# Kernel tuning notes

Hardware: AMD Instinct MI355X
Metric: run time of the kernel (lower is better)

Reference implementation:

```python
import jax, jax.numpy as jnp
import numpy as np

N = 50000        # nodes
E = 800000       # edges (avg degree 16)
C_IN = 128
H = 256          # hidden_channels
C_OUT = 128
DEPTH = 4
K = 2            # k_hops -> K+1 = 3 TAGConv weight matrices
L = DEPTH - 1    # residual layers after layer-0 conv
EPS = 1e-5
SLOPE = 0.01     # LeakyReLU default negative slope


def setup_inputs() -> dict:
    key = jax.random.key(0)
    ks = iter(jax.random.split(key, 24))
    s = 0.02
    x = jax.random.normal(next(ks), (N, C_IN), dtype=jnp.float32)
    edge_index = jax.random.randint(next(ks), (2, E), 0, N, dtype=jnp.int64)
    edge_weight = jax.random.uniform(next(ks), (E,), dtype=jnp.float32)
    return {
        'x': x,
        'edge_index': edge_index,
        'edge_weight': edge_weight,
        'W_emb': jax.random.normal(next(ks), (C_IN, H)) * s,
        'b_emb': jnp.zeros((H,), jnp.float32),
        'conv0_W': jax.random.normal(next(ks), (K + 1, H, H)) * s,
        'conv0_b': jnp.zeros((H,), jnp.float32),
        'norm_g': jnp.ones((L, H), jnp.float32),
        'norm_b': jnp.zeros((L, H), jnp.float32),
        'conv_W': jax.random.normal(next(ks), (L, K + 1, H, H)) * s,
        'conv_b': jnp.zeros((L, H), jnp.float32),
        'mlp_W1': jax.random.normal(next(ks), (L, H, 4 * H)) * s,
        'mlp_b1': jnp.zeros((L, 4 * H), jnp.float32),
        'mlp_g': jnp.ones((L, 4 * H), jnp.float32),
        'mlp_bb': jnp.zeros((L, 4 * H), jnp.float32),
        'mlp_W2': jax.random.normal(next(ks), (L, 4 * H, H)) * s,
        'mlp_b2': jnp.zeros((L, H), jnp.float32),
        'W_out': jax.random.normal(next(ks), (H, C_OUT)) * s,
        'b_out': jnp.zeros((C_OUT,), jnp.float32),
    }


def _bn(h, g, b):
    # BatchNorm1d over node dim (training-mode batch statistics)
    m = h.mean(axis=0)
    v = h.var(axis=0)
    return g * (h - m) * jax.lax.rsqrt(v + EPS) + b


def _tagconv(h, src, dst, ew, Ws, b):
    # TAGConv (normalize=False, no self loops): sum_k (A^k h) W_k + b
    out = h @ Ws[0]
    p = h
    for k in range(1, Ws.shape[0]):
        msg = p[src] * ew[:, None]                      # [E, H] gather
        p = jax.ops.segment_sum(msg, dst, num_segments=h.shape[0])
        out = out + p @ Ws[k]
    return out + b


def reference(x, edge_index, edge_weight, W_emb, b_emb, conv0_W, conv0_b,
              norm_g, norm_b, conv_W, conv_b, mlp_W1, mlp_b1, mlp_g, mlp_bb,
              mlp_W2, mlp_b2, W_out, b_out):
    src, dst = edge_index[0], edge_index[1]
    h = x @ W_emb + b_emb                               # x_embed (t=None)
    h = _tagconv(h, src, dst, edge_weight, conv0_W, conv0_b)  # layer-0 conv only
    for l in range(norm_g.shape[0]):                    # res+ blocks
        z = jax.nn.leaky_relu(_bn(h, norm_g[l], norm_b[l]), SLOPE)
        z = _tagconv(z, src, dst, edge_weight, conv_W[l], conv_b[l])
        # pyg MLP [H, 4H, H]: Linear -> BN -> act -> Linear (plain last)
        z = jax.nn.leaky_relu(_bn(z @ mlp_W1[l] + mlp_b1[l], mlp_g[l], mlp_bb[l]), SLOPE)
        z = z @ mlp_W2[l] + mlp_b2[l]
        h = h + z                                       # residual (res=Identity)
    return h @ W_out + b_out
```

## Files before the change

kernel.cpp:

```cpp
#include <hip/hip_runtime.h>

#define HDIM 256
#define EPSV 1e-5f
#define SLOPEV 0.01f

typedef __bf16 bf16;
typedef bf16  bf16x8 __attribute__((ext_vector_type(8)));
typedef bf16  bf16x4 __attribute__((ext_vector_type(4)));
typedef float f32x4  __attribute__((ext_vector_type(4)));

#define GLD16(g, l) __builtin_amdgcn_global_load_lds( \
    (const __attribute__((address_space(1))) void*)(g), \
    (__attribute__((address_space(3))) void*)(l), 16, 0, 0)

template<bool STORE_BF16>
__global__ __launch_bounds__(256)
void gemm_bt_k(const bf16* A0, const bf16* A1, const bf16* A2, const bf16* A3,
               int nseg, int segK,
               const bf16* __restrict__ Wt,
               const float* __restrict__ bias, const bf16* __restrict__ addb,
               void* out0, void* out1, void* out2, void* out3, int ldo,
               int n_store, float* part, int n_stats)
{
    __shared__ char smem[17408];
    bf16* As = (bf16*)smem;
    bf16* Bs = (bf16*)(smem + 8192);

    const int tid = threadIdx.x;
    const int wave = tid >> 6, lane = tid & 63;
    const int quad = lane >> 4, l16 = lane & 15;
    const int waveM = (wave >> 1) * 64, waveN = (wave & 1) * 64;
    const int bm = blockIdx.y * 128, bn = blockIdx.x * 128;
    const int K = nseg * segK;

    const bf16* segs[4] = {A0, A1, A2, A3};
    char* lA0 = (char*)As + wave * 1024;
    char* lA1 = (char*)As + 4096 + wave * 1024;
    char* lB0 = (char*)Bs + wave * 1024;
    char* lB1 = (char*)Bs + 4096 + wave * 1024;
    const bf16* pa = As + (waveM + l16) * 32 + quad * 8;
    const bf16* pb = Bs + (waveN + l16) * 32 + quad * 8;

    f32x4 acc[4][4] = {};

    for (int s = 0; s < nseg; ++s) {
        const bf16* A = segs[s];
        const bf16* gA0 = A + (size_t)(bm + (tid >> 2)) * segK + (tid & 3) * 8;
        const bf16* gA1 = A + (size_t)(bm + 64 + (tid >> 2)) * segK + (tid & 3) * 8;
        const bf16* gB0 = Wt + (size_t)(bn + (tid >> 2)) * K + s * segK + (tid & 3) * 8;
        const bf16* gB1 = Wt + (size_t)(bn + 64 + (tid >> 2)) * K + s * segK + (tid & 3) * 8;
        for (int kt = 0; kt < segK; kt += 32) {
            GLD16(gA0, lA0); GLD16(gA1, lA1);
            GLD16(gB0, lB0); GLD16(gB1, lB1);
            gA0 += 32; gA1 += 32; gB0 += 32; gB1 += 32;
            __syncthreads();

            bf16x8 a0 = *(const bf16x8*)(pa);
            bf16x8 a1 = *(const bf16x8*)(pa + 16 * 32);
            bf16x8 a2 = *(const bf16x8*)(pa + 32 * 32);
            bf16x8 a3 = *(const bf16x8*)(pa + 48 * 32);
            bf16x8 b0 = *(const bf16x8*)(pb);
            bf16x8 b1 = *(const bf16x8*)(pb + 16 * 32);
            bf16x8 b2 = *(const bf16x8*)(pb + 32 * 32);
            bf16x8 b3 = *(const bf16x8*)(pb + 48 * 32);

            acc[0][0] = __builtin_amdgcn_mfma_f32_16x16x32_bf16(a0, b0, acc[0][0], 0, 0, 0);
            acc[0][1] = __builtin_amdgcn_mfma_f32_16x16x32_bf16(a0, b1, acc[0][1], 0, 0, 0);
            acc[0][2] = __builtin_amdgcn_mfma_f32_16x16x32_bf16(a0, b2, acc[0][2], 0, 0, 0);
            acc[0][3] = __builtin_amdgcn_mfma_f32_16x16x32_bf16(a0, b3, acc[0][3], 0, 0, 0);
            acc[1][0] = __builtin_amdgcn_mfma_f32_16x16x32_bf16(a1, b0, acc[1][0], 0, 0, 0);
            acc[1][1] = __builtin_amdgcn_mfma_f32_16x16x32_bf16(a1, b1, acc[1][1], 0, 0, 0);
            acc[1][2] = __builtin_amdgcn_mfma_f32_16x16x32_bf16(a1, b2, acc[1][2], 0, 0, 0);
            acc[1][3] = __builtin_amdgcn_mfma_f32_16x16x32_bf16(a1, b3, acc[1][3], 0, 0, 0);
            acc[2][0] = __builtin_amdgcn_mfma_f32_16x16x32_bf16(a2, b0, acc[2][0], 0, 0, 0);
            acc[2][1] = __builtin_amdgcn_mfma_f32_16x16x32_bf16(a2, b1, acc[2][1], 0, 0, 0);
            acc[2][2] = __builtin_amdgcn_mfma_f32_16x16x32_bf16(a2, b2, acc[2][2], 0, 0, 0);
            acc[2][3] = __builtin_amdgcn_mfma_f32_16x16x32_bf16(a2, b3, acc[2][3], 0, 0, 0);
            acc[3][0] = __builtin_amdgcn_mfma_f32_16x16x32_bf16(a3, b0, acc[3][0], 0, 0, 0);
            acc[3][1] = __builtin_amdgcn_mfma_f32_16x16x32_bf16(a3, b1, acc[3][1], 0, 0, 0);
            acc[3][2] = __builtin_amdgcn_mfma_f32_16x16x32_bf16(a3, b2, acc[3][2], 0, 0, 0);
            acc[3][3] = __builtin_amdgcn_mfma_f32_16x16x32_bf16(a3, b3, acc[3][3], 0, 0, 0);
            __syncthreads();
        }
    }

    float bv[4];
#pragma unroll
    for (int j = 0; j < 4; ++j)
        bv[j] = bias ? bias[bn + waveN + j * 16 + l16] : 0.f;
#pragma unroll
    for (int i = 0; i < 4; ++i)
#pragma unroll
        for (int j = 0; j < 4; ++j)
#pragma unroll
            for (int r = 0; r < 4; ++r)
                acc[i][j][r] += bv[j];

    void* outs[4] = {out0, out1, out2, out3};

    if (STORE_BF16) {
        char* stg = smem + wave * 4352;
        float s8[8] = {}, q8[8] = {};
        const int rsel = lane >> 3, csel = lane & 7;
#pragma unroll
        for (int ih = 0; ih < 2; ++ih) {
            __syncthreads();
#pragma unroll
            for (int iw = 0; iw < 2; ++iw) {
                int i = ih * 2 + iw;
#pragma unroll
                for (int j = 0; j < 4; ++j)
#pragma unroll
                    for (int r = 0; r < 4; ++r)
                        *(bf16*)(stg + ((iw * 16 + quad * 4 + r) * 68 + j * 16 + l16) * 2)
                            = (bf16)acc[i][j][r];
            }
            __syncthreads();
#pragma unroll
            for (int rr = 0; rr < 4; ++rr) {
                int rl = rsel + rr * 8;
                bf16x4 lo = *(const bf16x4*)(stg + (rl * 68 + csel * 8) * 2);
                bf16x4 hi = *(const bf16x4*)(stg + (rl * 68 + csel * 8 + 4) * 2);
                int rowg = bm + waveM + ih * 32 + rl;
                int colg = bn + waveN + csel * 8;
                int cseg = colg >> 8, cloc = colg & 255;
                size_t idx = (size_t)rowg * ldo + cloc;
                float f[8];
#pragma unroll
                for (int u = 0; u < 4; ++u) { f[u] = (float)lo[u]; f[4 + u] = (float)hi[u]; }
                if (addb) {
                    bf16x8 o = *(const bf16x8*)(addb + idx);
#pragma unroll
                    for (int u = 0; u < 8; ++u) f[u] += (float)o[u];
                }
                bf16x8 w;
#pragma unroll
                for (int u = 0; u < 8; ++u) w[u] = (bf16)f[u];
                if (rowg < n_store) *(bf16x8*)((bf16*)outs[cseg] + idx) = w;
                if (part && rowg < n_stats) {
#pragma unroll
                    for (int u = 0; u < 8; ++u) { s8[u] += f[u]; q8[u] += f[u] * f[u]; }
                }
            }
        }
        if (part) {
#pragma unroll
            for (int m = 8; m <= 32; m <<= 1)
#pragma unroll
                for (int u = 0; u < 8; ++u) {
                    s8[u] += __shfl_xor(s8[u], m, 64);
                    q8[u] += __shfl_xor(q8[u], m, 64);
                }
            __syncthreads();
            float* Ls = (float*)smem;
            float* Lq = Ls + 256;
            if (rsel == 0) {
#pragma unroll
                for (int u = 0; u < 8; ++u) {
                    Ls[wave * 64 + csel * 8 + u] = s8[u];
                    Lq[wave * 64 + csel * 8 + u] = q8[u];
                }
            }
            __syncthreads();
            if (tid < 128) {
                int hi = tid >> 6, c6 = tid & 63;
                float s = Ls[hi * 64 + c6] + Ls[(hi + 2) * 64 + c6];
                float q = Lq[hi * 64 + c6] + Lq[(hi + 2) * 64 + c6];
                int Mtot = gridDim.x * 128;
                int colg = bn + tid;
                part[(size_t)blockIdx.y * Mtot + colg] = s;
                part[(size_t)(gridDim.y + blockIdx.y) * Mtot + colg] = q;
            }
        }
    } else {
#pragma unroll
        for (int i = 0; i < 4; ++i)
#pragma unroll
            for (int j = 0; j < 4; ++j) {
                int colg = bn + waveN + j * 16 + l16;
                int cseg = colg >> 8, cloc = colg & 255;
#pragma unroll
                for (int r = 0; r < 4; ++r) {
                    int rowg = bm + waveM + i * 16 + quad * 4 + r;
                    if (rowg < n_store)
                        ((float*)outs[cseg])[(size_t)rowg * ldo + cloc] = acc[i][j][r];
                }
            }
    }
}

__global__ __launch_bounds__(256)
void finalize_k(const float* __restrict__ part, int GY, int M,
                const float* __restrict__ g, const float* __restrict__ bb,
                float* __restrict__ coef, float invn)
{
    const int c = blockIdx.x;
    const int t = threadIdx.x;
    float s = 0.f, q = 0.f;
    const float* ps = part + c;
    const float* pq = part + (size_t)GY * M + c;
    for (int i = t; i < GY; i += 256) {
        s += ps[(size_t)i * M];
        q += pq[(size_t)i * M];
    }
#pragma unroll
    for (int m = 1; m <= 32; m <<= 1) {
        s += __shfl_xor(s, m, 64);
        q += __shfl_xor(q, m, 64);
    }
    __shared__ float Ls[4], Lq[4];
    const int w = t >> 6, l = t & 63;
    if (l == 0) { Ls[w] = s; Lq[w] = q; }
    __syncthreads();
    if (t == 0) {
        s = Ls[0] + Ls[1] + Ls[2] + Ls[3];
        q = Lq[0] + Lq[1] + Lq[2] + Lq[3];
        float mean = s * invn;
        float var  = q * invn - mean * mean;
        float a = g[c] * rsqrtf(var + EPSV);
        coef[c]     = a;
        coef[M + c] = bb[c] - mean * a;
    }
}

__global__ __launch_bounds__(256)
void transpose_cvt_k(const float* __restrict__ src, bf16* __restrict__ dst,
                     int Kseg, int M, int G)
{
    __shared__ float t[32][33];
    const int z = blockIdx.z;
    src += (size_t)z * Kseg * M;
    const int ldd = G * Kseg;
    dst += (size_t)(z / G) * M * ldd + (size_t)(z % G) * Kseg;
    const int tM = blockIdx.x * 32, tK = blockIdx.y * 32;
    const int tx = threadIdx.x & 31, ty = threadIdx.x >> 5;
#pragma unroll
    for (int r = 0; r < 4; ++r)
        t[ty + r * 8][tx] = src[(size_t)(tK + ty + r * 8) * M + tM + tx];
    __syncthreads();
#pragma unroll
    for (int r = 0; r < 4; ++r)
        dst[(size_t)(tM + ty + r * 8) * ldd + tK + tx] = (bf16)t[tx][ty + r * 8];
}

__global__ __launch_bounds__(256)
void cvt_bf_k(const float* __restrict__ src, bf16* __restrict__ dst, long n4)
{
    long i = (long)blockIdx.x * blockDim.x + threadIdx.x;
    if (i >= n4) return;
    float4 v = ((const float4*)src)[i];
    bf16x4 o; o[0] = (bf16)v.x; o[1] = (bf16)v.y; o[2] = (bf16)v.z; o[3] = (bf16)v.w;
    ((bf16x4*)dst)[i] = o;
}

__global__ __launch_bounds__(256)
void deg_k(const int* __restrict__ dst, int* __restrict__ deg, int E)
{
    int e = blockIdx.x * blockDim.x + threadIdx.x;
    if (e < E) atomicAdd(&deg[dst[e]], 1);
}

__global__ __launch_bounds__(1024)
void scan_k(int* __restrict__ deg_wp, int* __restrict__ rowptr, int N)
{
    __shared__ int s[1024];
    const int tid = threadIdx.x;
    if (tid == 0) rowptr[0] = 0;
    int running = 0;
    for (int base = 0; base < N; base += 1024) {
        int i = base + tid;
        int x = (i < N) ? deg_wp[i] : 0;
        s[tid] = x;
        __syncthreads();
        for (int off = 1; off < 1024; off <<= 1) {
            int t = (tid >= off) ? s[tid - off] : 0;
            __syncthreads();
            s[tid] += t;
            __syncthreads();
        }
        if (i < N) {
            rowptr[i + 1] = s[tid] + running;
            deg_wp[i]     = s[tid] + running - x;
        }
        running += s[1023];
        __syncthreads();
    }
}

__global__ __launch_bounds__(256)
void reorder_k(const int* __restrict__ src, const int* __restrict__ dst,
               const float* __restrict__ ew, int* __restrict__ wp,
               int* __restrict__ col, float* __restrict__ wgt, int E)
{
    int e = blockIdx.x * blockDim.x + threadIdx.x;
    if (e >= E) return;
    int d = dst[e];
    int pos = atomicAdd(&wp[d], 1);
    col[pos] = src[e];
    wgt[pos] = ew[e];
}

__global__ __launch_bounds__(256)
void spmm_pull_k(const bf16* __restrict__ P, const int* __restrict__ rowptr,
                 const int* __restrict__ col, const float* __restrict__ wgt,
                 bf16* __restrict__ Q, int N)
{
    int node = blockIdx.x * 8 + (threadIdx.x >> 5);
    int l = threadIdx.x & 31;
    if (node >= N) return;
    int e = rowptr[node], end = rowptr[node + 1];
    float acc[8] = {};
    for (; e + 1 < end; e += 2) {
        int   s0 = col[e], s1 = col[e + 1];
        float w0 = wgt[e], w1 = wgt[e + 1];
        bf16x8 v0 = *(const bf16x8*)(P + (size_t)s0 * HDIM + l * 8);
        bf16x8 v1 = *(const bf16x8*)(P + (size_t)s1 * HDIM + l * 8);
#pragma unroll
        for (int u = 0; u < 8; ++u)
            acc[u] += (float)v0[u] * w0 + (float)v1[u] * w1;
    }
    if (e < end) {
        int s0 = col[e]; float w0 = wgt[e];
        bf16x8 v0 = *(const bf16x8*)(P + (size_t)s0 * HDIM + l * 8);
#pragma unroll
        for (int u = 0; u < 8; ++u) acc[u] += (float)v0[u] * w0;
    }
    bf16x8 o;
#pragma unroll
    for (int u = 0; u < 8; ++u) o[u] = (bf16)acc[u];
    *(bf16x8*)(Q + (size_t)node * HDIM + l * 8) = o;
}

__global__ __launch_bounds__(256)
void apply_bn_k(const bf16* __restrict__ X, const float* __restrict__ coef,
                bf16* __restrict__ Y, int n)
{
    __shared__ float aL[256], bL[256];
    const int tid = threadIdx.x;
    aL[tid] = coef[tid]; bL[tid] = coef[256 + tid];
    __syncthreads();
    long n4 = (long)n * 64;
    for (long i = (long)blockIdx.x * 256 + tid; i < n4; i += (long)gridDim.x * 256) {
        bf16x4 v = ((const bf16x4*)X)[i];
        int c4 = (int)(i & 63) * 4;
        float r0 = fmaf((float)v[0], aL[c4 + 0], bL[c4 + 0]); r0 = r0 > 0.f ? r0 : SLOPEV * r0;
        float r1 = fmaf((float)v[1], aL[c4 + 1], bL[c4 + 1]); r1 = r1 > 0.f ? r1 : SLOPEV * r1;
        float r2 = fmaf((float)v[2], aL[c4 + 2], bL[c4 + 2]); r2 = r2 > 0.f ? r2 : SLOPEV * r2;
        float r3 = fmaf((float)v[3], aL[c4 + 3], bL[c4 + 3]); r3 = r3 > 0.f ? r3 : SLOPEV * r3;
        bf16x4 o; o[0] = (bf16)r0; o[1] = (bf16)r1; o[2] = (bf16)r2; o[3] = (bf16)r3;
        ((bf16x4*)Y)[i] = o;
    }
}

__global__ __launch_bounds__(256)
void apply_bn4_k(bf16* X0, bf16* X1, bf16* X2, bf16* X3,
                 const float* __restrict__ coef, int n)
{
    __shared__ float aL[1024], bL[1024];
    const int tid = threadIdx.x;
#pragma unroll
    for (int q = 0; q < 4; ++q) {
        int c = q * 256 + tid;
        aL[c] = coef[c]; bL[c] = coef[1024 + c];
    }
    __syncthreads();
    bf16* Xs[4] = {X0, X1, X2, X3};
    long per = (long)n * 64;
    long stride = (long)gridDim.x * 256;
    for (int q = 0; q < 4; ++q) {
        bf16* X = Xs[q];
        int cbase = q * 256;
        for (long i = (long)blockIdx.x * 256 + tid; i < per; i += stride) {
            bf16x4 v = ((const bf16x4*)X)[i];
            int c4 = cbase + (int)(i & 63) * 4;
            float r0 = fmaf((float)v[0], aL[c4 + 0], bL[c4 + 0]); r0 = r0 > 0.f ? r0 : SLOPEV * r0;
            float r1 = fmaf((float)v[1], aL[c4 + 1], bL[c4 + 1]); r1 = r1 > 0.f ? r1 : SLOPEV * r1;
            float r2 = fmaf((float)v[2], aL[c4 + 2], bL[c4 + 2]); r2 = r2 > 0.f ? r2 : SLOPEV * r2;
            float r3 = fmaf((float)v[3], aL[c4 + 3], bL[c4 + 3]); r3 = r3 > 0.f ? r3 : SLOPEV * r3;
            bf16x4 o; o[0] = (bf16)r0; o[1] = (bf16)r1; o[2] = (bf16)r2; o[3] = (bf16)r3;
            ((bf16x4*)X)[i] = o;
        }
    }
}

struct GemmArgs {
    const bf16 *A0, *A1, *A2, *A3; int nseg, segK;
    const bf16* Wt; const float* bias; const bf16* addb;
    void *o0, *o1, *o2, *o3; int ldo, M, n_store;
    float* part; int n_stats;
};

static void gemm(hipStream_t st, const GemmArgs& a, int GY, bool store_bf16)
{
    dim3 g(a.M / 128, GY), b(256);
    if (store_bf16)
        gemm_bt_k<true><<<g, b, 0, st>>>(a.A0, a.A1, a.A2, a.A3, a.nseg, a.segK,
            a.Wt, a.bias, a.addb, a.o0, a.o1, a.o2, a.o3, a.ldo, a.n_store,
            a.part, a.n_stats);
    else
        gemm_bt_k<false><<<g, b, 0, st>>>(a.A0, a.A1, a.A2, a.A3, a.nseg, a.segK,
            a.Wt, a.bias, a.addb, a.o0, a.o1, a.o2, a.o3, a.ldo, a.n_store,
            a.part, a.n_stats);
}

extern "C" void kernel_launch(void* const* d_in, const int* in_sizes, int n_in,
                              void* d_out, int out_size, void* d_ws, size_t ws_size,
                              hipStream_t stream)
{
    const float* x       = (const float*)d_in[0];
    const int*   ei      = (const int*)d_in[1];
    const float* ew      = (const float*)d_in[2];
    const float* W_emb   = (const float*)d_in[3];
    const float* b_emb   = (const float*)d_in[4];
    const float* conv0_W = (const float*)d_in[5];
    const float* conv0_b = (const float*)d_in[6];
    const float* norm_g  = (const float*)d_in[7];
    const float* norm_b  = (const float*)d_in[8];
    const float* conv_W  = (const float*)d_in[9];
    const float* conv_b  = (const float*)d_in[10];
    const float* mlp_W1  = (const float*)d_in[11];
    const float* mlp_b1  = (const float*)d_in[12];
    const float* mlp_g   = (const float*)d_in[13];
    const float* mlp_bb  = (const float*)d_in[14];
    const float* mlp_W2  = (const float*)d_in[15];
    const float* mlp_b2  = (const float*)d_in[16];
    const float* W_out   = (const float*)d_in[17];
    const float* b_out   = (const float*)d_in[18];

    const int N = in_sizes[0] / 128;
    const int E = in_sizes[2];
    const int* srcI = ei;
    const int* dstI = ei + E;
    const int N_pad = ((N + 127) / 128) * 128;
    const int GY = N_pad / 128;

    const size_t NHp = (size_t)N_pad * HDIM;
    bf16* xb = (bf16*)d_ws;
    bf16* hb = xb + (size_t)N_pad * 128;
    bf16* cb = hb + NHp;
    bf16* p1 = cb + NHp;
    bf16* p2 = p1 + NHp;
    bf16* e1 = p2 + NHp;
    bf16* e2 = e1 + NHp;
    bf16* wa = e2 + NHp;
    bf16* Wt_emb   = wa;
    bf16* Wt_conv0 = wa + 32768;
    bf16* Wt_conv  = wa + 229376;
    bf16* Wt_mlp1  = wa + 819200;
    bf16* Wt_mlp2  = wa + 1605632;
    bf16* Wt_out   = wa + 2392064;
    float* cf_h   = (float*)(wa + 2424832);
    float* cf_m   = cf_h + 512;
    float* partb  = cf_m + 2048;
    int*   rowptr = (int*)(partb + 2 * (size_t)GY * 1024);
    int*   wp     = rowptr + (N + 1);
    int*   col    = wp + N;
    float* wgt    = (float*)(col + E);

    const float invn = 1.0f / (float)N;
    dim3 pg((N + 7) / 8), pb(256);

    hipMemsetAsync(wp, 0, (size_t)N * 4, stream);
    deg_k<<<dim3((E + 255) / 256), dim3(256), 0, stream>>>(dstI, wp, E);
    scan_k<<<dim3(1), dim3(1024), 0, stream>>>(wp, rowptr, N);
    reorder_k<<<dim3((E + 255) / 256), dim3(256), 0, stream>>>(srcI, dstI, ew, wp, col, wgt, E);

    cvt_bf_k<<<dim3((N * 32 + 255) / 256), dim3(256), 0, stream>>>(x, xb, (long)N * 32);
    transpose_cvt_k<<<dim3(8, 4, 1), dim3(256), 0, stream>>>(W_emb, Wt_emb, 128, 256, 1);
    transpose_cvt_k<<<dim3(8, 8, 3), dim3(256), 0, stream>>>(conv0_W, Wt_conv0, 256, 256, 3);
    transpose_cvt_k<<<dim3(8, 8, 9), dim3(256), 0, stream>>>(conv_W, Wt_conv, 256, 256, 3);
    transpose_cvt_k<<<dim3(32, 8, 3), dim3(256), 0, stream>>>(mlp_W1, Wt_mlp1, 256, 1024, 1);
    transpose_cvt_k<<<dim3(8, 32, 3), dim3(256), 0, stream>>>(mlp_W2, Wt_mlp2, 1024, 256, 1);
    transpose_cvt_k<<<dim3(4, 8, 1), dim3(256), 0, stream>>>(W_out, Wt_out, 256, 128, 1);

    {
        GemmArgs a{xb, xb, xb, xb, 1, 128, Wt_emb, b_emb, nullptr,
                   cb, cb, cb, cb, HDIM, 256, N_pad, nullptr, 0};
        gemm(stream, a, GY, true);
    }

    spmm_pull_k<<<pg, pb, 0, stream>>>(cb, rowptr, col, wgt, p1, N);
    spmm_pull_k<<<pg, pb, 0, stream>>>(p1, rowptr, col, wgt, p2, N);
    {
        GemmArgs a{cb, p1, p2, p2, 3, 256, Wt_conv0, conv0_b, nullptr,
                   hb, hb, hb, hb, HDIM, 256, N_pad, partb, N};
        gemm(stream, a, GY, true);
    }
    finalize_k<<<dim3(256), dim3(256), 0, stream>>>(partb, GY, 256, norm_g, norm_b, cf_h, invn);

    for (int l = 0; l < 3; ++l) {
        apply_bn_k<<<dim3(1024), dim3(256), 0, stream>>>(hb, cf_h, e1, N);

        spmm_pull_k<<<pg, pb, 0, stream>>>(e1, rowptr, col, wgt, p1, N);
        spmm_pull_k<<<pg, pb, 0, stream>>>(p1, rowptr, col, wgt, p2, N);
        {
            GemmArgs a{e1, p1, p2, p2, 3, 256, Wt_conv + (size_t)l * 196608,
                       conv_b + l * 256, nullptr, cb, cb, cb, cb, HDIM, 256, N_pad,
                       nullptr, 0};
            gemm(stream, a, GY, true);
        }

        {
            GemmArgs a{cb, cb, cb, cb, 1, 256, Wt_mlp1 + (size_t)l * 262144,
                       mlp_b1 + (size_t)l * 1024, nullptr, p1, p2, e1, e2, HDIM, 1024,
                       N_pad, partb, N};
            gemm(stream, a, GY, true);
        }
        finalize_k<<<dim3(1024), dim3(256), 0, stream>>>(partb, GY, 1024,
                                                         mlp_g + (size_t)l * 1024,
                                                         mlp_bb + (size_t)l * 1024, cf_m, invn);

        apply_bn4_k<<<dim3(2048), dim3(256), 0, stream>>>(p1, p2, e1, e2, cf_m, N);

        {
            GemmArgs a{p1, p2, e1, e2, 4, 256, Wt_mlp2 + (size_t)l * 262144,
                       mlp_b2 + l * 256, hb, hb, hb, hb, hb, HDIM, 256, N_pad,
                       (l < 2) ? partb : nullptr, N};
            gemm(stream, a, GY, true);
        }
        if (l < 2)
            finalize_k<<<dim3(256), dim3(256), 0, stream>>>(partb, GY, 256,
                                                            norm_g + (l + 1) * 256,
                                                            norm_b + (l + 1) * 256, cf_h, invn);
    }

    {
        GemmArgs a{hb, hb, hb, hb, 1, 256, Wt_out, b_out, nullptr,
                   d_out, d_out, d_out, d_out, 128, 128, N, nullptr, 0};
        gemm(stream, a, GY, false);
    }
}
```

Measured before the change: 1.543 ms.

## Deepen GEMM K-tile to 64 and parallelize CSR prefix scan across blocks

The GEMM main loop now stages a 64-wide K slice per iteration, with eight async global-to-LDS loads per thread and two MFMA sub-steps between barriers, halving barrier count per K. Shared memory grows from about 17 KB to 32 KB. The single-block 1024-thread degree scan, which loops serially over all nodes, is replaced by a three-kernel block-sum, top-scan and scatter-scan. This removes a long serial launch, though the top scan handles at most 256 blocks, which covers N=50000 but not larger graphs.

```diff
diff --git a/kernel.cpp b/kernel.cpp
--- a/kernel.cpp
+++ b/kernel.cpp
@@ -22,9 +22,9 @@
                void* out0, void* out1, void* out2, void* out3, int ldo,
                int n_store, float* part, int n_stats)
 {
-    __shared__ char smem[17408];
+    __shared__ char smem[32768];
     bf16* As = (bf16*)smem;
-    bf16* Bs = (bf16*)(smem + 8192);
+    bf16* Bs = (bf16*)(smem + 16384);
 
     const int tid = threadIdx.x;
     const int wave = tid >> 6, lane = tid & 63;
@@ -34,52 +34,62 @@
     const int K = nseg * segK;
 
     const bf16* segs[4] = {A0, A1, A2, A3};
-    char* lA0 = (char*)As + wave * 1024;
-    char* lA1 = (char*)As + 4096 + wave * 1024;
-    char* lB0 = (char*)Bs + wave * 1024;
-    char* lB1 = (char*)Bs + 4096 + wave * 1024;
-    const bf16* pa = As + (waveM + l16) * 32 + quad * 8;
-    const bf16* pb = Bs + (waveN + l16) * 32 + quad * 8;
+    const int srow = tid >> 3;
+    const int skof = (tid & 7) * 8;
+    char* lA = (char*)As + wave * 1024;
+    char* lB = (char*)Bs + wave * 1024;
+    const bf16* pa = As + (waveM + l16) * 64 + quad * 8;
+    const bf16* pb = Bs + (waveN + l16) * 64 + quad * 8;
 
     f32x4 acc[4][4] = {};
 
     for (int s = 0; s < nseg; ++s) {
-        const bf16* A = segs[s];
-        const bf16* gA0 = A + (size_t)(bm + (tid >> 2)) * segK + (tid & 3) * 8;
-        const bf16* gA1 = A + (size_t)(bm + 64 + (tid >> 2)) * segK + (tid & 3) * 8;
-        const bf16* gB0 = Wt + (size_t)(bn + (tid >> 2)) * K + s * segK + (tid & 3) * 8;
-        const bf16* gB1 = Wt + (size_t)(bn + 64 + (tid >> 2)) * K + s * segK + (tid & 3) * 8;
-        for (int kt = 0; kt < segK; kt += 32) {
-            GLD16(gA0, lA0); GLD16(gA1, lA1);
-            GLD16(gB0, lB0); GLD16(gB1, lB1);
-            gA0 += 32; gA1 += 32; gB0 += 32; gB1 += 32;
+        const bf16* gA = segs[s] + (size_t)(bm + srow) * segK + skof;
+        const bf16* gB = Wt + (size_t)(bn + srow) * K + s * segK + skof;
+        const size_t offA = (size_t)32 * segK;
+        const size_t offB = (size_t)32 * K;
+        for (int kt = 0; kt < segK; kt += 64) {
+            GLD16(gA,            lA);
+            GLD16(gA + offA,     lA + 4096);
+            GLD16(gA + 2 * offA, lA + 8192);
+            GLD16(gA + 3 * offA, lA + 12288);
+            GLD16(gB,            lB);
+            GLD16(gB + offB,     lB + 4096);
+            GLD16(gB + 2 * offB, lB + 8192);
+            GLD16(gB + 3 * offB, lB + 12288);
+            gA += 64; gB += 64;
             __syncthreads();
 
-            bf16x8 a0 = *(const bf16x8*)(pa);
-            bf16x8 a1 = *(const bf16x8*)(pa + 16 * 32);
-            bf16x8 a2 = *(const bf16x8*)(pa + 32 * 32);
-            bf16x8 a3 = *(const bf16x8*)(pa + 48 * 32);
-            bf16x8 b0 = *(const bf16x8*)(pb);
-            bf16x8 b1 = *(const bf16x8*)(pb + 16 * 32);
-            bf16x8 b2 = *(const bf16x8*)(pb + 32 * 32);
-            bf16x8 b3 = *(const bf16x8*)(pb + 48 * 32);
-
-            acc[0][0] = __builtin_amdgcn_mfma_f32_16x16x32_bf16(a0, b0, acc[0][0], 0, 0, 0);
-            acc[0][1] = __builtin_amdgcn_mfma_f32_16x16x32_bf16(a0, b1, acc[0][1], 0, 0, 0);
-            acc[0][2] = __builtin_amdgcn_mfma_f32_16x16x32_bf16(a0, b2, acc[0][2], 0, 0, 0);
-            acc[0][3] = __builtin_amdgcn_mfma_f32_16x16x32_bf16(a0, b3, acc[0][3], 0, 0, 0);
-            acc[1][0] = __builtin_amdgcn_mfma_f32_16x16x32_bf16(a1, b0, acc[1][0], 0, 0, 0);
-            acc[1][1] = __builtin_amdgcn_mfma_f32_16x16x32_bf16(a1, b1, acc[1][1], 0, 0, 0);
-            acc[1][2] = __builtin_amdgcn_mfma_f32_16x16x32_bf16(a1, b2, acc[1][2], 0, 0, 0);
-            acc[1][3] = __builtin_amdgcn_mfma_f32_16x16x32_bf16(a1, b3, acc[1][3], 0, 0, 0);
-            acc[2][0] = __builtin_amdgcn_mfma_f32_16x16x32_bf16(a2, b0, acc[2][0], 0, 0, 0);
-            acc[2][1] = __builtin_amdgcn_mfma_f32_16x16x32_bf16(a2, b1, acc[2][1], 0, 0, 0);
-            acc[2][2] = __builtin_amdgcn_mfma_f32_16x16x32_bf16(a2, b2, acc[2][2], 0, 0, 0);
-            acc[2][3] = __builtin_amdgcn_mfma_f32_16x16x32_bf16(a2, b3, acc[2][3], 0, 0, 0);
-            acc[3][0] = __builtin_amdgcn_mfma_f32_16x16x32_bf16(a3, b0, acc[3][0], 0, 0, 0);
-            acc[3][1] = __builtin_amdgcn_mfma_f32_16x16x32_bf16(a3, b1, acc[3][1], 0, 0, 0);
-            acc[3][2] = __builtin_amdgcn_mfma_f32_16x16x32_bf16(a3, b2, acc[3][2], 0, 0, 0);
-            acc[3][3] = __builtin_amdgcn_mfma_f32_16x16x32_bf16(a3, b3, acc[3][3], 0, 0, 0);
+#pragma unroll
+            for (int ks = 0; ks < 2; ++ks) {
+                const bf16* pak = pa + ks * 32;
+                const bf16* pbk = pb + ks * 32;
+                bf16x8 a0 = *(const bf16x8*)(pak);
+                bf16x8 a1 = *(const bf16x8*)(pak + 16 * 64);
+                bf16x8 a2 = *(const bf16x8*)(pak + 32 * 64);
+                bf16x8 a3 = *(const bf16x8*)(pak + 48 * 64);
+                bf16x8 b0 = *(const bf16x8*)(pbk);
+                bf16x8 b1 = *(const bf16x8*)(pbk + 16 * 64);
+                bf16x8 b2 = *(const bf16x8*)(pbk + 32 * 64);
+                bf16x8 b3 = *(const bf16x8*)(pbk + 48 * 64);
+
+                acc[0][0] = __builtin_amdgcn_mfma_f32_16x16x32_bf16(a0, b0, acc[0][0], 0, 0, 0);
+                acc[0][1] = __builtin_amdgcn_mfma_f32_16x16x32_bf16(a0, b1, acc[0][1], 0, 0, 0);
+                acc[0][2] = __builtin_amdgcn_mfma_f32_16x16x32_bf16(a0, b2, acc[0][2], 0, 0, 0);
+                acc[0][3] = __builtin_amdgcn_mfma_f32_16x16x32_bf16(a0, b3, acc[0][3], 0, 0, 0);
+                acc[1][0] = __builtin_amdgcn_mfma_f32_16x16x32_bf16(a1, b0, acc[1][0], 0, 0, 0);
+                acc[1][1] = __builtin_amdgcn_mfma_f32_16x16x32_bf16(a1, b1, acc[1][1], 0, 0, 0);
+                acc[1][2] = __builtin_amdgcn_mfma_f32_16x16x32_bf16(a1, b2, acc[1][2], 0, 0, 0);
+                acc[1][3] = __builtin_amdgcn_mfma_f32_16x16x32_bf16(a1, b3, acc[1][3], 0, 0, 0);
+                acc[2][0] = __builtin_amdgcn_mfma_f32_16x16x32_bf16(a2, b0, acc[2][0], 0, 0, 0);
+                acc[2][1] = __builtin_amdgcn_mfma_f32_16x16x32_bf16(a2, b1, acc[2][1], 0, 0, 0);
+                acc[2][2] = __builtin_amdgcn_mfma_f32_16x16x32_bf16(a2, b2, acc[2][2], 0, 0, 0);
+                acc[2][3] = __builtin_amdgcn_mfma_f32_16x16x32_bf16(a2, b3, acc[2][3], 0, 0, 0);
+                acc[3][0] = __builtin_amdgcn_mfma_f32_16x16x32_bf16(a3, b0, acc[3][0], 0, 0, 0);
+                acc[3][1] = __builtin_amdgcn_mfma_f32_16x16x32_bf16(a3, b1, acc[3][1], 0, 0, 0);
+                acc[3][2] = __builtin_amdgcn_mfma_f32_16x16x32_bf16(a3, b2, acc[3][2], 0, 0, 0);
+                acc[3][3] = __builtin_amdgcn_mfma_f32_16x16x32_bf16(a3, b3, acc[3][3], 0, 0, 0);
+            }
             __syncthreads();
         }
     }
@@ -260,30 +270,57 @@
     if (e < E) atomicAdd(&deg[dst[e]], 1);
 }
 
-__global__ __launch_bounds__(1024)
-void scan_k(int* __restrict__ deg_wp, int* __restrict__ rowptr, int N)
-{
-    __shared__ int s[1024];
-    const int tid = threadIdx.x;
-    if (tid == 0) rowptr[0] = 0;
-    int running = 0;
-    for (int base = 0; base < N; base += 1024) {
-        int i = base + tid;
-        int x = (i < N) ? deg_wp[i] : 0;
-        s[tid] = x;
+__global__ __launch_bounds__(256)
+void blocksum_k(const int* __restrict__ deg, int* __restrict__ bsum, int N)
+{
+    int i = blockIdx.x * 256 + threadIdx.x;
+    int v = (i < N) ? deg[i] : 0;
+#pragma unroll
+    for (int m = 1; m <= 32; m <<= 1) v += __shfl_xor(v, m, 64);
+    __shared__ int Ls[4];
+    if ((threadIdx.x & 63) == 0) Ls[threadIdx.x >> 6] = v;
+    __syncthreads();
+    if (threadIdx.x == 0) bsum[blockIdx.x] = Ls[0] + Ls[1] + Ls[2] + Ls[3];
+}
+
+__global__ __launch_bounds__(256)
+void topscan_k(const int* __restrict__ bsum, int* __restrict__ boff, int nb)
+{
+    __shared__ int s[256];
+    int t = threadIdx.x;
+    int v = (t < nb) ? bsum[t] : 0;
+    s[t] = v;
+    __syncthreads();
+    for (int off = 1; off < 256; off <<= 1) {
+        int u = (t >= off) ? s[t - off] : 0;
         __syncthreads();
-        for (int off = 1; off < 1024; off <<= 1) {
-            int t = (tid >= off) ? s[tid - off] : 0;
-            __syncthreads();
-            s[tid] += t;
-            __syncthreads();
-        }
-        if (i < N) {
-            rowptr[i + 1] = s[tid] + running;
-            deg_wp[i]     = s[tid] + running - x;
-        }
-        running += s[1023];
+        s[t] += u;
         __syncthreads();
+    }
+    if (t < nb) boff[t] = s[t] - v;
+}
+
+__global__ __launch_bounds__(256)
+void scatterscan_k(int* __restrict__ deg_wp, const int* __restrict__ boff,
+                   int* __restrict__ rowptr, int N)
+{
+    __shared__ int s[256];
+    int t = threadIdx.x;
+    int i = blockIdx.x * 256 + t;
+    int v = (i < N) ? deg_wp[i] : 0;
+    s[t] = v;
+    __syncthreads();
+    for (int off = 1; off < 256; off <<= 1) {
+        int u = (t >= off) ? s[t - off] : 0;
+        __syncthreads();
+        s[t] += u;
+        __syncthreads();
+    }
+    if (i < N) {
+        int incl = s[t] + boff[blockIdx.x];
+        rowptr[i + 1] = incl;
+        deg_wp[i] = incl - v;
+        if (i == 0) rowptr[0] = 0;
     }
 }
 
@@ -433,6 +470,7 @@
     const int* dstI = ei + E;
     const int N_pad = ((N + 127) / 128) * 128;
     const int GY = N_pad / 128;
+    const int NB = (N + 255) / 256;
 
     const size_t NHp = (size_t)N_pad * HDIM;
     bf16* xb = (bf16*)d_ws;
@@ -456,13 +494,17 @@
     int*   wp     = rowptr + (N + 1);
     int*   col    = wp + N;
     float* wgt    = (float*)(col + E);
+    int*   bsum   = (int*)(wgt + E);
+    int*   boff   = bsum + 256;
 
     const float invn = 1.0f / (float)N;
     dim3 pg((N + 7) / 8), pb(256);
 
     hipMemsetAsync(wp, 0, (size_t)N * 4, stream);
     deg_k<<<dim3((E + 255) / 256), dim3(256), 0, stream>>>(dstI, wp, E);
-    scan_k<<<dim3(1), dim3(1024), 0, stream>>>(wp, rowptr, N);
+    blocksum_k<<<dim3(NB), dim3(256), 0, stream>>>(wp, bsum, N);
+    topscan_k<<<dim3(1), dim3(256), 0, stream>>>(bsum, boff, NB);
+    scatterscan_k<<<dim3(NB), dim3(256), 0, stream>>>(wp, boff, rowptr, N);
     reorder_k<<<dim3((E + 255) / 256), dim3(256), 0, stream>>>(srcI, dstI, ew, wp, col, wgt, E);
 
     cvt_bf_k<<<dim3((N * 32 + 255) / 256), dim3(256), 0, stream>>>(x, xb, (long)N * 32);
```

After: 1.489 ms. 3.5% less time.
